# Optimization experiments

Measured on AMD Instinct MI355X. Metric: run time of the kernel, lower is better.

## Reference

```python
import jax, jax.numpy as jnp
import numpy as np

SCALING = 16.0 / 16.0  # lora_alpha / r

def setup_inputs() -> dict:
    key = jax.random.key(0)
    k1, k2, k3, k4, k5 = jax.random.split(key, 5)
    B, S, D, R = 4, 4096, 4096, 16
    x = jax.random.normal(k1, (B, S, D), dtype=jnp.float32)
    W = jax.random.normal(k2, (D, D), dtype=jnp.float32) * (1.0 / np.sqrt(D))
    bias = jax.random.normal(k3, (D,), dtype=jnp.float32) * 0.02
    lora_A = jax.random.normal(k4, (D, R), dtype=jnp.float32) * (1.0 / np.sqrt(D))
    lora_B = jax.random.normal(k5, (R, D), dtype=jnp.float32) * 0.02
    return {"x": x, "W": W, "bias": bias, "lora_A": lora_A, "lora_B": lora_B}

def reference(x, W, bias, lora_A, lora_B):
    x_dtype = x.dtype
    # base (quantized) linear modeled as dense GEMM: [B,S,D] @ [D,D]
    out = jnp.einsum('bsd,df->bsf', x, W)
    # low-rank LoRA path: (x @ A) @ B * scaling, computed in train_dtype then cast back
    lora = jnp.einsum('bsr,rf->bsf', jnp.einsum('bsd,dr->bsr', x.astype(lora_A.dtype), lora_A), lora_B) * SCALING
    out = out + lora.astype(x_dtype)
    out = out + bias.astype(x_dtype)
    return out
```

## Files before the change

### kernel.cpp

```cpp
#include <hip/hip_runtime.h>
#include <hip/hip_bf16.h>


typedef __attribute__((ext_vector_type(8))) __bf16 bf16x8;
typedef __attribute__((ext_vector_type(4))) float f32x4;

#define M_DIM 16384
#define N_DIM 4096
#define K_DIM 4096

__device__ __forceinline__ void async16(const void* g, void* l) {
    __builtin_amdgcn_global_load_lds((const __attribute__((address_space(1))) void*)g,
                                     (__attribute__((address_space(3))) void*)l,
                                     16, 0, 0);
}

__global__ void cast_x_kernel(const float* __restrict__ x, __bf16* __restrict__ xb, size_t n) {
    size_t i0 = ((size_t)blockIdx.x * blockDim.x + threadIdx.x) * 8;
    size_t stride = (size_t)gridDim.x * blockDim.x * 8;
    for (size_t i = i0; i < n; i += stride) {
        f32x4 v0 = __builtin_nontemporal_load((const f32x4*)(x + i));
        f32x4 v1 = __builtin_nontemporal_load((const f32x4*)(x + i + 4));
        bf16x8 o;
        o[0] = (__bf16)v0[0]; o[1] = (__bf16)v0[1]; o[2] = (__bf16)v0[2]; o[3] = (__bf16)v0[3];
        o[4] = (__bf16)v1[0]; o[5] = (__bf16)v1[1]; o[6] = (__bf16)v1[2]; o[7] = (__bf16)v1[3];
        *(bf16x8*)(xb + i) = o;
    }
}

__global__ void prep_w_kernel(const float* __restrict__ W, const float* __restrict__ A,
                              const float* __restrict__ Bm, __bf16* __restrict__ Wt) {
    __shared__ float Ws[32][33];
    __shared__ float As[32][16];
    __shared__ float Bs[16][32];
    const int tx = threadIdx.x;
    const int ty = threadIdx.y;
    const int t = ty * 32 + tx;
    const int n0 = blockIdx.x * 32;
    const int k0 = blockIdx.y * 32;

#pragma unroll
    for (int i = 0; i < 4; ++i) {
        int k = ty + i * 8;
        Ws[k][tx] = W[(size_t)(k0 + k) * N_DIM + n0 + tx];
    }
    for (int i = t; i < 512; i += 256)
        As[i >> 4][i & 15] = A[(size_t)(k0 + (i >> 4)) * 16 + (i & 15)];
    for (int i = t; i < 512; i += 256)
        Bs[i >> 5][i & 31] = Bm[(size_t)(i >> 5) * N_DIM + n0 + (i & 31)];
    __syncthreads();

    float a[16];
#pragma unroll
    for (int r = 0; r < 16; ++r) a[r] = As[tx][r];
#pragma unroll
    for (int i = 0; i < 4; ++i) {
        int n = ty + i * 8;
        float acc = Ws[tx][n];
#pragma unroll
        for (int r = 0; r < 16; ++r) acc += a[r] * Bs[r][n];
        Wt[(size_t)(n0 + n) * K_DIM + k0 + tx] = (__bf16)acc;
    }
}


#define WAIT_VM(N) asm volatile("s_waitcnt vmcnt(" #N ")" ::: "memory")
#define BARRIER() do { asm volatile("" ::: "memory"); __builtin_amdgcn_s_barrier(); asm volatile("" ::: "memory"); } while (0)

#define ST(ptr, koff, ldsbase, row0) \
    async16((ptr) + (koff), (ldsbase) + (row0) * 128 + sldsoff)

#define LOAD_AF(ldsbase, MH)                                                         \
    _Pragma("unroll") for (int m_ = 0; m_ < 4; ++m_)                                 \
    _Pragma("unroll") for (int ks_ = 0; ks_ < 2; ++ks_)                              \
        afr[m_][ks_] = *(const bf16x8*)((ldsbase) + aRowB + (MH) * 8192 + m_ * 2048 + colsw[ks_]);

#define LOAD_BF(dst, ldsbase, NH)                                                    \
    _Pragma("unroll") for (int n_ = 0; n_ < 2; ++n_)                                 \
    _Pragma("unroll") for (int ks_ = 0; ks_ < 2; ++ks_)                              \
        dst[n_][ks_] = *(const bf16x8*)((ldsbase) + bRowB + (NH) * 16384 + n_ * 2048 + colsw[ks_]);

#define MFMA_Q(MH, NH, BF)                                                           \
    __builtin_amdgcn_s_setprio(1);                                                   \
    _Pragma("unroll") for (int m_ = 0; m_ < 4; ++m_)                                 \
    _Pragma("unroll") for (int n_ = 0; n_ < 2; ++n_)                                 \
    _Pragma("unroll") for (int ks_ = 0; ks_ < 2; ++ks_)                              \
        acc[(MH) * 4 + m_][(NH) * 2 + n_] = __builtin_amdgcn_mfma_f32_16x16x32_bf16( \
            afr[m_][ks_], BF[n_][ks_], acc[(MH) * 4 + m_][(NH) * 2 + n_], 0, 0, 0);  \
    __builtin_amdgcn_s_setprio(0);                                                   \
    __builtin_amdgcn_sched_barrier(0);

#define TILE_FULL(AC, BC, AO, BO, KT)                                                \
    LOAD_AF(AC, 0); LOAD_BF(b0f, BC, 0);                                             \
    ST(pB0, (KT) + 64, BO, 0);    ST(pB1, (KT) + 64, BO, 64);                        \
    BARRIER(); MFMA_Q(0, 0, b0f);                                                    \
    LOAD_BF(b1f, BC, 1);                                                             \
    ST(pA1, (KT) + 64, AO, 64);   ST(pA3, (KT) + 64, AO, 192);                       \
    BARRIER(); MFMA_Q(0, 1, b1f); WAIT_VM(8);                                        \
    LOAD_AF(AC, 1);                                                                  \
    ST(pA0, (KT) + 128, AC, 0);   ST(pA2, (KT) + 128, AC, 128);                      \
    BARRIER(); MFMA_Q(1, 1, b1f);                                                    \
    ST(pB2, (KT) + 128, BC, 128); ST(pB3, (KT) + 128, BC, 192);                      \
    BARRIER(); MFMA_Q(1, 0, b0f); WAIT_VM(6);

__global__ __launch_bounds__(512, 2) void gemm256_kernel(
    const __bf16* __restrict__ Xb, const __bf16* __restrict__ Wt,
    const float* __restrict__ bias, float* __restrict__ out) {
    extern __shared__ __align__(16) char smem[];
    const int tid  = threadIdx.x;
    const int lane = tid & 63;
    const int wave = tid >> 6;
    const int wr = wave >> 2;
    const int wn = wave & 3;

    const int bid = blockIdx.x;
    const int wg = (bid & 7) * 128 + (bid >> 3);
    const int m0 = (wg >> 4) * 256;
    const int n0 = (wg & 15) * 256;

    char* A0 = smem;
    char* B0 = smem + 32768;
    char* A1 = smem + 65536;
    char* B1 = smem + 98304;

    const int srow = tid >> 3;
    const int scol = ((tid & 7) ^ (srow & 7)) << 3;
    const int sldsoff = wave * 1024;

    const __bf16* pA0 = Xb + (size_t)(m0 + 0   + srow) * K_DIM + scol;
    const __bf16* pA1 = Xb + (size_t)(m0 + 64  + srow) * K_DIM + scol;
    const __bf16* pA2 = Xb + (size_t)(m0 + 128 + srow) * K_DIM + scol;
    const __bf16* pA3 = Xb + (size_t)(m0 + 192 + srow) * K_DIM + scol;
#define BPERM(P) ((((P) >> 5) & 3) * 64 + (((P) >> 7) & 1) * 32 + ((P) & 31))
    const __bf16* pB0 = Wt + (size_t)(n0 + BPERM(0   + srow)) * K_DIM + scol;
    const __bf16* pB1 = Wt + (size_t)(n0 + BPERM(64  + srow)) * K_DIM + scol;
    const __bf16* pB2 = Wt + (size_t)(n0 + BPERM(128 + srow)) * K_DIM + scol;
    const __bf16* pB3 = Wt + (size_t)(n0 + BPERM(192 + srow)) * K_DIM + scol;

    int colsw[2];
#pragma unroll
    for (int ks = 0; ks < 2; ++ks)
        colsw[ks] = ((ks * 32 + (lane >> 4) * 8) ^ ((lane & 7) * 8)) << 1;
    const int aRowB = (wr * 128 + (lane & 15)) * 128;
    const int bRowB = (wn * 32 + (lane & 15)) * 128;

    f32x4 acc[8][4] = {};
    bf16x8 afr[4][2], b0f[2][2], b1f[2][2];

    ST(pA0, 0, A0, 0);    ST(pA2, 0, A0, 128);
    ST(pB0, 0, B0, 0);    ST(pB1, 0, B0, 64);
    ST(pA1, 0, A0, 64);   ST(pA3, 0, A0, 192);
    ST(pB2, 0, B0, 128);  ST(pB3, 0, B0, 192);
    ST(pA0, 64, A1, 0);   ST(pA2, 64, A1, 128);
    ST(pB2, 64, B1, 128); ST(pB3, 64, B1, 192);
    WAIT_VM(4);
    BARRIER();

    for (int it = 0; it < 31; ++it) {
        const int kt = it * 128;
        TILE_FULL(A0, B0, A1, B1, kt);
        TILE_FULL(A1, B1, A0, B0, kt + 64);
    }

    LOAD_AF(A0, 0); LOAD_BF(b0f, B0, 0);
    ST(pB0, 4032, B1, 0); ST(pB1, 4032, B1, 64);
    BARRIER(); MFMA_Q(0, 0, b0f);
    LOAD_BF(b1f, B0, 1);
    ST(pA1, 4032, A1, 64); ST(pA3, 4032, A1, 192);
    BARRIER(); MFMA_Q(0, 1, b1f); WAIT_VM(8);
    LOAD_AF(A0, 1);
    BARRIER(); MFMA_Q(1, 1, b1f);
    BARRIER(); MFMA_Q(1, 0, b0f); WAIT_VM(0);

    LOAD_AF(A1, 0); LOAD_BF(b0f, B1, 0);
    BARRIER(); MFMA_Q(0, 0, b0f);
    LOAD_BF(b1f, B1, 1);
    BARRIER(); MFMA_Q(0, 1, b1f);
    LOAD_AF(A1, 1);
    BARRIER(); MFMA_Q(1, 1, b1f);
    MFMA_Q(1, 0, b0f);

#pragma unroll
    for (int mh = 0; mh < 2; ++mh)
#pragma unroll
        for (int m = 0; m < 4; ++m) {
            const int gr = m0 + wr * 128 + mh * 64 + m * 16 + (lane >> 4) * 4;
#pragma unroll
            for (int nh = 0; nh < 2; ++nh)
#pragma unroll
                for (int n = 0; n < 2; ++n) {
                    const int gc = n0 + wn * 64 + nh * 32 + n * 16 + (lane & 15);
                    const float bv = bias[gc];
                    const f32x4 a = acc[mh * 4 + m][nh * 2 + n];
#pragma unroll
                    for (int j = 0; j < 4; ++j)
                        __builtin_nontemporal_store(a[j] + bv,
                            &out[(size_t)(gr + j) * N_DIM + gc]);
                }
        }
}

extern "C" void kernel_launch(void* const* d_in, const int* in_sizes, int n_in,
                              void* d_out, int out_size, void* d_ws, size_t ws_size,
                              hipStream_t stream) {
    const float* x    = (const float*)d_in[0];
    const float* W    = (const float*)d_in[1];
    const float* bias = (const float*)d_in[2];
    const float* lA   = (const float*)d_in[3];
    const float* lB   = (const float*)d_in[4];
    float* out = (float*)d_out;

    __bf16* Xb = (__bf16*)d_ws;
    __bf16* Wt = (__bf16*)((char*)d_ws + (size_t)M_DIM * K_DIM * 2);

    cast_x_kernel<<<2048, 256, 0, stream>>>(x, Xb, (size_t)M_DIM * K_DIM);
    prep_w_kernel<<<dim3(N_DIM / 32, K_DIM / 32), dim3(32, 8), 0, stream>>>(W, lA, lB, Wt);

    (void)hipFuncSetAttribute((const void*)gemm256_kernel,
                              hipFuncAttributeMaxDynamicSharedMemorySize, 131072);
    gemm256_kernel<<<1024, 512, 131072, stream>>>(Xb, Wt, bias, out);
}
```

Measured before the change: 545.9 us.

## Double-buffer A fragments and reorder LDS reads ahead of MFMA quadrants

Splits the A-fragment register buffer into two (afr0/afr1) so the next tile's first A fragment is read from LDS during the current tile's last MFMA quadrant. All B fragments are loaded up front, and barriers and vmcnt waits are moved after each MFMA block instead of before it. The aim is to hide LDS read latency behind matrix math and cut per-quadrant stalls. The cost is extra VGPRs for the second A buffer, which could pressure the 2-blocks-per-CU occupancy target, and the reworked barrier and wait placement must still guard the LDS buffer reuse correctly.

```diff
diff --git a/kernel.cpp b/kernel.cpp
--- a/kernel.cpp
+++ b/kernel.cpp
@@ -70,38 +70,38 @@
 #define ST(ptr, koff, ldsbase, row0) \
     async16((ptr) + (koff), (ldsbase) + (row0) * 128 + sldsoff)
 
-#define LOAD_AF(ldsbase, MH)                                                         \
+#define LOAD_AFd(dst, ldsbase, MH)                                                   \
     _Pragma("unroll") for (int m_ = 0; m_ < 4; ++m_)                                 \
     _Pragma("unroll") for (int ks_ = 0; ks_ < 2; ++ks_)                              \
-        afr[m_][ks_] = *(const bf16x8*)((ldsbase) + aRowB + (MH) * 8192 + m_ * 2048 + colsw[ks_]);
+        dst[m_][ks_] = *(const bf16x8*)((ldsbase) + aRowB + (MH) * 8192 + m_ * 2048 + colsw[ks_]);
 
 #define LOAD_BF(dst, ldsbase, NH)                                                    \
     _Pragma("unroll") for (int n_ = 0; n_ < 2; ++n_)                                 \
     _Pragma("unroll") for (int ks_ = 0; ks_ < 2; ++ks_)                              \
         dst[n_][ks_] = *(const bf16x8*)((ldsbase) + bRowB + (NH) * 16384 + n_ * 2048 + colsw[ks_]);
 
-#define MFMA_Q(MH, NH, BF)                                                           \
+#define MFMA_Q(AF, MB, NB, BF)                                                       \
     __builtin_amdgcn_s_setprio(1);                                                   \
     _Pragma("unroll") for (int m_ = 0; m_ < 4; ++m_)                                 \
     _Pragma("unroll") for (int n_ = 0; n_ < 2; ++n_)                                 \
     _Pragma("unroll") for (int ks_ = 0; ks_ < 2; ++ks_)                              \
-        acc[(MH) * 4 + m_][(NH) * 2 + n_] = __builtin_amdgcn_mfma_f32_16x16x32_bf16( \
-            afr[m_][ks_], BF[n_][ks_], acc[(MH) * 4 + m_][(NH) * 2 + n_], 0, 0, 0);  \
+        acc[(MB) + m_][(NB) + n_] = __builtin_amdgcn_mfma_f32_16x16x32_bf16(         \
+            AF[m_][ks_], BF[n_][ks_], acc[(MB) + m_][(NB) + n_], 0, 0, 0);           \
     __builtin_amdgcn_s_setprio(0);                                                   \
     __builtin_amdgcn_sched_barrier(0);
 
-#define TILE_FULL(AC, BC, AO, BO, KT)                                                \
-    LOAD_AF(AC, 0); LOAD_BF(b0f, BC, 0);                                             \
+#define TILE_P(AC, BC, AO, BO, KT)                                                   \
+    LOAD_BF(b0f, BC, 0); LOAD_BF(b1f, BC, 1);                                        \
     ST(pB0, (KT) + 64, BO, 0);    ST(pB1, (KT) + 64, BO, 64);                        \
-    BARRIER(); MFMA_Q(0, 0, b0f);                                                    \
-    LOAD_BF(b1f, BC, 1);                                                             \
+    MFMA_Q(afr0, 0, 0, b0f); WAIT_VM(6); BARRIER();                                  \
+    LOAD_AFd(afr1, AC, 1);                                                           \
     ST(pA1, (KT) + 64, AO, 64);   ST(pA3, (KT) + 64, AO, 192);                       \
-    BARRIER(); MFMA_Q(0, 1, b1f); WAIT_VM(8);                                        \
-    LOAD_AF(AC, 1);                                                                  \
+    MFMA_Q(afr0, 0, 2, b1f); BARRIER();                                              \
     ST(pA0, (KT) + 128, AC, 0);   ST(pA2, (KT) + 128, AC, 128);                      \
-    BARRIER(); MFMA_Q(1, 1, b1f);                                                    \
+    MFMA_Q(afr1, 4, 2, b1f); BARRIER();                                              \
     ST(pB2, (KT) + 128, BC, 128); ST(pB3, (KT) + 128, BC, 192);                      \
-    BARRIER(); MFMA_Q(1, 0, b0f); WAIT_VM(6);
+    LOAD_AFd(afr0, AO, 0);                                                           \
+    MFMA_Q(afr1, 4, 0, b0f); WAIT_VM(6); BARRIER();
 
 __global__ __launch_bounds__(512, 2) void gemm256_kernel(
     const __bf16* __restrict__ Xb, const __bf16* __restrict__ Wt,
@@ -145,7 +145,7 @@
     const int bRowB = (wn * 32 + (lane & 15)) * 128;
 
     f32x4 acc[8][4] = {};
-    bf16x8 afr[4][2], b0f[2][2], b1f[2][2];
+    bf16x8 afr0[4][2], afr1[4][2], b0f[2][2], b1f[2][2];
 
     ST(pA0, 0, A0, 0);    ST(pA2, 0, A0, 128);
     ST(pB0, 0, B0, 0);    ST(pB1, 0, B0, 64);
@@ -155,30 +155,31 @@
     ST(pB2, 64, B1, 128); ST(pB3, 64, B1, 192);
     WAIT_VM(4);
     BARRIER();
+    LOAD_AFd(afr0, A0, 0);
 
     for (int it = 0; it < 31; ++it) {
         const int kt = it * 128;
-        TILE_FULL(A0, B0, A1, B1, kt);
-        TILE_FULL(A1, B1, A0, B0, kt + 64);
-    }
-
-    LOAD_AF(A0, 0); LOAD_BF(b0f, B0, 0);
+        TILE_P(A0, B0, A1, B1, kt);
+        TILE_P(A1, B1, A0, B0, kt + 64);
+    }
+
+    LOAD_BF(b0f, B0, 0); LOAD_BF(b1f, B0, 1);
     ST(pB0, 4032, B1, 0); ST(pB1, 4032, B1, 64);
-    BARRIER(); MFMA_Q(0, 0, b0f);
-    LOAD_BF(b1f, B0, 1);
+    MFMA_Q(afr0, 0, 0, b0f); WAIT_VM(6); BARRIER();
+    LOAD_AFd(afr1, A0, 1);
     ST(pA1, 4032, A1, 64); ST(pA3, 4032, A1, 192);
-    BARRIER(); MFMA_Q(0, 1, b1f); WAIT_VM(8);
-    LOAD_AF(A0, 1);
-    BARRIER(); MFMA_Q(1, 1, b1f);
-    BARRIER(); MFMA_Q(1, 0, b0f); WAIT_VM(0);
-
-    LOAD_AF(A1, 0); LOAD_BF(b0f, B1, 0);
-    BARRIER(); MFMA_Q(0, 0, b0f);
-    LOAD_BF(b1f, B1, 1);
-    BARRIER(); MFMA_Q(0, 1, b1f);
-    LOAD_AF(A1, 1);
-    BARRIER(); MFMA_Q(1, 1, b1f);
-    MFMA_Q(1, 0, b0f);
+    MFMA_Q(afr0, 0, 2, b1f); BARRIER();
+    MFMA_Q(afr1, 4, 2, b1f); BARRIER();
+    WAIT_VM(6);
+    LOAD_AFd(afr0, A1, 0);
+    MFMA_Q(afr1, 4, 0, b0f); WAIT_VM(0); BARRIER();
+
+    LOAD_BF(b0f, B1, 0); LOAD_BF(b1f, B1, 1);
+    MFMA_Q(afr0, 0, 0, b0f);
+    LOAD_AFd(afr1, A1, 1);
+    MFMA_Q(afr0, 0, 2, b1f);
+    MFMA_Q(afr1, 4, 2, b1f);
+    MFMA_Q(afr1, 4, 0, b0f);
 
 #pragma unroll
     for (int mh = 0; mh < 2; ++mh)
```

Measured after the change: 1.028 ms. +88.4%, slower.
